# Optimization experiments

Hardware: AMD Instinct MI355X
Metric: run time of the kernel (lower is better)

The kernel has to match this reference:

```python
import jax, jax.numpy as jnp
import numpy as np

N = 100000   # num_nodes
E = 1250000  # num_edges
IN = 64
HID = 64
OUT = 64
LN_EPS = 1e-5


def _gcn_conv(x, src, dst, W, b, n):
    # PyG GCNConv: add self-loops, symmetric deg^{-1/2} normalization, then linear.
    h = x @ W  # (N, out)
    deg = jax.ops.segment_sum(jnp.ones(src.shape[0], h.dtype), dst, num_segments=n) + 1.0  # +1 self-loop
    dinv = jax.lax.rsqrt(deg)
    norm = dinv[src] * dinv[dst]  # (E,)
    out = jax.ops.segment_sum(h[src] * norm[:, None], dst, num_segments=n)
    out = out + h * (dinv * dinv)[:, None]  # self-loop message
    return out + b


def _sage_conv(x, src, dst, Wl, bl, Wr, n):
    # PyG SAGEConv(aggr='mean'): lin_l(mean_{j in N(i)} x_j) + lin_r(x_i); bias only in lin_l.
    cnt = jax.ops.segment_sum(jnp.ones(src.shape[0], x.dtype), dst, num_segments=n)
    agg = jax.ops.segment_sum(x[src], dst, num_segments=n) / jnp.maximum(cnt, 1.0)[:, None]
    return agg @ Wl + bl + x @ Wr


def _layer_norm(x, g, b):
    mu = jnp.mean(x, axis=-1, keepdims=True)
    var = jnp.var(x, axis=-1, keepdims=True)
    return (x - mu) * jax.lax.rsqrt(var + LN_EPS) * g + b


def setup_inputs() -> dict:
    key = jax.random.key(0)
    ks = jax.random.split(key, 16)
    def w(k, shape):
        fan_in = shape[0]
        return (jax.random.normal(k, shape, jnp.float32) / np.sqrt(fan_in)).astype(jnp.float32)
    x = jax.random.normal(ks[0], (N, IN), jnp.float32)
    edge_index = jax.random.randint(ks[1], (2, E), 0, N, dtype=jnp.int64)
    return {
        "x": x,
        "edge_index": edge_index,
        "gcn_w1": w(ks[2], (IN, HID)), "gcn_b1": jnp.zeros((HID,), jnp.float32),
        "gcn_w2": w(ks[3], (HID, OUT)), "gcn_b2": jnp.zeros((OUT,), jnp.float32),
        "sage_wl1": w(ks[4], (IN, HID)), "sage_bl1": jnp.zeros((HID,), jnp.float32),
        "sage_wr1": w(ks[5], (IN, HID)),
        "sage_wl2": w(ks[6], (HID, OUT)), "sage_bl2": jnp.zeros((OUT,), jnp.float32),
        "sage_wr2": w(ks[7], (HID, OUT)),
        "gcn_ln_g": jnp.ones((OUT,), jnp.float32), "gcn_ln_b": jnp.zeros((OUT,), jnp.float32),
        "sage_ln_g": jnp.ones((OUT,), jnp.float32), "sage_ln_b": jnp.zeros((OUT,), jnp.float32),
        "proj_w": w(ks[8], (2 * OUT, OUT)), "proj_b": jnp.zeros((OUT,), jnp.float32),
    }


def reference(x, edge_index, gcn_w1, gcn_b1, gcn_w2, gcn_b2,
              sage_wl1, sage_bl1, sage_wr1, sage_wl2, sage_bl2, sage_wr2,
              gcn_ln_g, gcn_ln_b, sage_ln_g, sage_ln_b, proj_w, proj_b):
    src, dst = edge_index[0], edge_index[1]
    n = x.shape[0]
    # GCN branch (dropout p=0 / eval -> identity)
    g = jax.nn.relu(_gcn_conv(x, src, dst, gcn_w1, gcn_b1, n))
    g = _gcn_conv(g, src, dst, gcn_w2, gcn_b2, n)
    # SAGE branch
    s = jax.nn.relu(_sage_conv(x, src, dst, sage_wl1, sage_bl1, sage_wr1, n))
    s = _sage_conv(s, src, dst, sage_wl2, sage_bl2, sage_wr2, n)
    # Norm + projected-concat fusion
    g = _layer_norm(g, gcn_ln_g, gcn_ln_b)
    s = _layer_norm(s, sage_ln_g, sage_ln_b)
    cat = jnp.concatenate([g, s], axis=-1)  # (N, 2*OUT)
    return cat @ proj_w + proj_b
```

## Files before the change

kernel.cpp:

```cpp
#include <hip/hip_runtime.h>


#define SCAN_CHUNK 2048

typedef __attribute__((ext_vector_type(8))) short short8;
typedef __attribute__((ext_vector_type(4))) short short4v;
typedef __attribute__((ext_vector_type(4))) float floatx4;

__device__ __forceinline__ unsigned short f2bf(float f) {
    unsigned int u = __float_as_uint(f);
    unsigned int r = u + 0x7FFFu + ((u >> 16) & 1u);
    return (unsigned short)(r >> 16);
}
__device__ __forceinline__ float bf2f(unsigned short h) {
    return __uint_as_float(((unsigned int)h) << 16);
}

__device__ __forceinline__ unsigned lds_addr(const void* p) {
    return (unsigned)(unsigned long long)(__attribute__((address_space(3))) const char*)p;
}

__device__ __forceinline__ short8 cat44(short4v lo, short4v hi) {
    short8 r;
    r[0] = lo[0]; r[1] = lo[1]; r[2] = lo[2]; r[3] = lo[3];
    r[4] = hi[0]; r[5] = hi[1]; r[6] = hi[2]; r[7] = hi[3];
    return r;
}

template<int NF, int CTB>
__device__ __forceinline__ void tr_read4(unsigned a0, short8 bf[4]) {
    short4v l0, h0, l1, h1, l2, h2, l3, h3;
    asm volatile(
        "ds_read_b64_tr_b16 %0, %8 offset:%9\n\t"
        "ds_read_b64_tr_b16 %1, %8 offset:%10\n\t"
        "ds_read_b64_tr_b16 %2, %8 offset:%11\n\t"
        "ds_read_b64_tr_b16 %3, %8 offset:%12\n\t"
        "ds_read_b64_tr_b16 %4, %8 offset:%13\n\t"
        "ds_read_b64_tr_b16 %5, %8 offset:%14\n\t"
        "ds_read_b64_tr_b16 %6, %8 offset:%15\n\t"
        "ds_read_b64_tr_b16 %7, %8 offset:%16\n\t"
        "s_waitcnt lgkmcnt(0)"
        : "=&v"(l0), "=&v"(h0), "=&v"(l1), "=&v"(h1),
          "=&v"(l2), "=&v"(h2), "=&v"(l3), "=&v"(h3)
        : "v"(a0),
          "i"((0 * NF + CTB + 0) * 128), "i"((1 * NF + CTB + 0) * 128),
          "i"((0 * NF + CTB + 1) * 128), "i"((1 * NF + CTB + 1) * 128),
          "i"((0 * NF + CTB + 2) * 128), "i"((1 * NF + CTB + 2) * 128),
          "i"((0 * NF + CTB + 3) * 128), "i"((1 * NF + CTB + 3) * 128)
        : "memory");
    bf[0] = cat44(l0, h0);
    bf[1] = cat44(l1, h1);
    bf[2] = cat44(l2, h2);
    bf[3] = cat44(l3, h3);
}

__global__ void k_count(const int* __restrict__ ei, int E, int* __restrict__ cnt,
                        int* __restrict__ rank,
                        const float* __restrict__ x, unsigned short* __restrict__ xb,
                        int xtotal, int do_x) {
    int i = blockIdx.x * blockDim.x + threadIdx.x;
    int e = i * 8;
    if (e + 8 <= E) {
        int4 d0 = *(const int4*)&ei[E + e];
        int4 d1 = *(const int4*)&ei[E + e + 4];
        int4 r0, r1;
        r0.x = atomicAdd(&cnt[d0.x], 1);
        r0.y = atomicAdd(&cnt[d0.y], 1);
        r0.z = atomicAdd(&cnt[d0.z], 1);
        r0.w = atomicAdd(&cnt[d0.w], 1);
        r1.x = atomicAdd(&cnt[d1.x], 1);
        r1.y = atomicAdd(&cnt[d1.y], 1);
        r1.z = atomicAdd(&cnt[d1.z], 1);
        r1.w = atomicAdd(&cnt[d1.w], 1);
        *(int4*)&rank[e] = r0;
        *(int4*)&rank[e + 4] = r1;
    } else if (e < E) {
        for (int j = e; j < E; ++j) rank[j] = atomicAdd(&cnt[ei[E + j]], 1);
    }
    if (do_x) {
        int xe = i * 8;
        if (xe + 8 <= xtotal) {
            float4 a = *(const float4*)&x[xe];
            float4 b = *(const float4*)&x[xe + 4];
            short8 o;
            o[0] = (short)f2bf(a.x); o[1] = (short)f2bf(a.y);
            o[2] = (short)f2bf(a.z); o[3] = (short)f2bf(a.w);
            o[4] = (short)f2bf(b.x); o[5] = (short)f2bf(b.y);
            o[6] = (short)f2bf(b.z); o[7] = (short)f2bf(b.w);
            *(short8*)&xb[xe] = o;
        } else if (xe < xtotal) {
            for (int j = xe; j < xtotal; ++j) xb[j] = f2bf(x[j]);
        }
    }
}

__global__ void k_scan_reduce(const int* __restrict__ cnt, int N, int* __restrict__ blockSums) {
    __shared__ int lds[256];
    int base = blockIdx.x * SCAN_CHUNK;
    int t = threadIdx.x;
    int s = 0;
    for (int j = 0; j < 8; ++j) {
        int idx = base + t * 8 + j;
        if (idx < N) s += cnt[idx] + 1;
    }
    lds[t] = s;
    __syncthreads();
    for (int d = 128; d > 0; d >>= 1) {
        if (t < d) lds[t] += lds[t + d];
        __syncthreads();
    }
    if (t == 0) blockSums[blockIdx.x] = lds[0];
}

__global__ void k_scan_spine(int* __restrict__ blockSums, int B) {
    if (threadIdx.x == 0 && blockIdx.x == 0) {
        int run = 0;
        for (int b = 0; b < B; ++b) { int v = blockSums[b]; blockSums[b] = run; run += v; }
    }
}

__global__ void k_scan_write(const int* __restrict__ cnt, int N,
                             const int* __restrict__ blockSums,
                             int* __restrict__ offs, float* __restrict__ dinv) {
    __shared__ int lds[256];
    int base = blockIdx.x * SCAN_CHUNK;
    int t = threadIdx.x;
    int v[8];
    int s = 0;
    for (int j = 0; j < 8; ++j) {
        int idx = base + t * 8 + j;
        v[j] = (idx < N) ? cnt[idx] : 0;
        s += (idx < N) ? v[j] + 1 : 0;
    }
    lds[t] = s;
    __syncthreads();
    for (int d = 1; d < 256; d <<= 1) {
        int x = (t >= d) ? lds[t - d] : 0;
        __syncthreads();
        lds[t] += x;
        __syncthreads();
    }
    int excl = (t == 0) ? 0 : lds[t - 1];
    int run = blockSums[blockIdx.x] + excl;
    for (int j = 0; j < 8; ++j) {
        int idx = base + t * 8 + j;
        if (idx < N) {
            offs[idx] = run;
            run += v[j] + 1;
            dinv[idx] = rsqrtf((float)v[j] + 1.0f);
            if (idx == N - 1) offs[N] = run;
        }
    }
}

__global__ void k_fill(const int* __restrict__ ei, int E, const int* __restrict__ offs,
                       const int* __restrict__ rank, const int* __restrict__ cnt,
                       const float* __restrict__ dinv,
                       int* __restrict__ csr, unsigned int* __restrict__ pk,
                       int use_pk, int N) {
    int i = blockIdx.x * blockDim.x + threadIdx.x;
    int e = i * 8;
    if (e + 8 <= E) {
        int4 s0 = *(const int4*)&ei[e];
        int4 s1 = *(const int4*)&ei[e + 4];
        int4 d0 = *(const int4*)&ei[E + e];
        int4 d1 = *(const int4*)&ei[E + e + 4];
        int4 r0 = *(const int4*)&rank[e];
        int4 r1 = *(const int4*)&rank[e + 4];
        int p0 = offs[d0.x] + r0.x, p1 = offs[d0.y] + r0.y;
        int p2 = offs[d0.z] + r0.z, p3 = offs[d0.w] + r0.w;
        int p4 = offs[d1.x] + r1.x, p5 = offs[d1.y] + r1.y;
        int p6 = offs[d1.z] + r1.z, p7 = offs[d1.w] + r1.w;
        csr[p0] = s0.x; csr[p1] = s0.y; csr[p2] = s0.z; csr[p3] = s0.w;
        csr[p4] = s1.x; csr[p5] = s1.y; csr[p6] = s1.z; csr[p7] = s1.w;
        if (use_pk) {
            pk[p0] = ((unsigned)(d0.x & 15) << 16) | f2bf(dinv[s0.x] * dinv[d0.x]);
            pk[p1] = ((unsigned)(d0.y & 15) << 16) | f2bf(dinv[s0.y] * dinv[d0.y]);
            pk[p2] = ((unsigned)(d0.z & 15) << 16) | f2bf(dinv[s0.z] * dinv[d0.z]);
            pk[p3] = ((unsigned)(d0.w & 15) << 16) | f2bf(dinv[s0.w] * dinv[d0.w]);
            pk[p4] = ((unsigned)(d1.x & 15) << 16) | f2bf(dinv[s1.x] * dinv[d1.x]);
            pk[p5] = ((unsigned)(d1.y & 15) << 16) | f2bf(dinv[s1.y] * dinv[d1.y]);
            pk[p6] = ((unsigned)(d1.z & 15) << 16) | f2bf(dinv[s1.z] * dinv[d1.z]);
            pk[p7] = ((unsigned)(d1.w & 15) << 16) | f2bf(dinv[s1.w] * dinv[d1.w]);
        }
    } else if (e < E) {
        for (int j = e; j < E; ++j) {
            int dd = ei[E + j];
            int p = offs[dd] + rank[j];
            csr[p] = ei[j];
            if (use_pk) pk[p] = ((unsigned)(dd & 15) << 16) | f2bf(dinv[ei[j]] * dinv[dd]);
        }
    }
    if (use_pk && i < N) {
        int pos = offs[i] + cnt[i];
        float di = dinv[i];
        csr[pos] = i;
        pk[pos] = ((unsigned)(i & 15) << 16) | (1u << 20) | f2bf(di * di);
    }
}

template<int ROWSH>
__launch_bounds__(256)
__global__ void k_gatherM(const unsigned short* __restrict__ feat,
                          const int* __restrict__ csr,
                          const unsigned int* __restrict__ pk,
                          const int* __restrict__ offs, const int* __restrict__ cnt,
                          unsigned short* __restrict__ agg, int N) {
    constexpr int NF = ROWSH / 16;
    constexpr int LPR = ROWSH / 8;
    constexpr int EPP = 64 / LPR;
    constexpr int PASSES = 32 / EPP;

    __shared__ unsigned short sbuf[4][32 * ROWSH];

    const int lane = threadIdx.x & 63;
    const int wv = threadIdx.x >> 6;
    const int base = blockIdx.x * 64 + wv * 16;
    if (base >= N) return;

    const int q = lane >> 4;
    const int d16 = lane & 15;

    const int parity = lane & 1;
    const int ei_low = (lane >> 1) & 3;
    const int sf_sub = (lane >> 3) & (NF - 1);
    const int ei_high = (NF == 8) ? 0 : (lane >> 5);
    const int eid = ei_high * 4 + ei_low;
    const int sf = sf_sub * 16 + parity * 8;

    const int elo = offs[base];
    const int ehi = offs[min(base + 16, N)];
    const int emax = ehi - 1;
    const int nch = (ehi - elo + 31) >> 5;

    int cM0, cM1, cM2, cM3;
    unsigned pM0, pM1, pM2, pM3;
    {
        int i0 = elo + lane;
        int i1 = i0 + 64, i2 = i0 + 128, i3 = i0 + 192;
        cM0 = csr[i0 <= emax ? i0 : emax];
        cM1 = csr[i1 <= emax ? i1 : emax];
        cM2 = csr[i2 <= emax ? i2 : emax];
        cM3 = csr[i3 <= emax ? i3 : emax];
        unsigned t0 = pk[i0 <= emax ? i0 : emax];
        unsigned t1 = pk[i1 <= emax ? i1 : emax];
        unsigned t2 = pk[i2 <= emax ? i2 : emax];
        unsigned t3 = pk[i3 <= emax ? i3 : emax];
        pM0 = (i0 < ehi) ? t0 : 0x00100000u;
        pM1 = (i1 < ehi) ? t1 : 0x00100000u;
        pM2 = (i2 < ehi) ? t2 : 0x00100000u;
        pM3 = (i3 < ehi) ? t3 : 0x00100000u;
    }

    floatx4 accg[4], accs[4];
#pragma unroll
    for (int i = 0; i < 4; ++i) {
        accg[i] = floatx4{0.f, 0.f, 0.f, 0.f};
        accs[i] = floatx4{0.f, 0.f, 0.f, 0.f};
    }

    unsigned short* wb = &sbuf[wv][0];
    const unsigned a0 = lds_addr(wb) + (unsigned)(q * 2 * NF) * 128u + (unsigned)d16 * 8u;

    for (int c = 0; c < nch; ++c) {
        int cv; unsigned pv; int wofs;
        int rc = c >> 1;
        if (rc < 4) {
            wofs = (c & 1) << 5;
            cv = (rc == 0) ? cM0 : (rc == 1) ? cM1 : (rc == 2) ? cM2 : cM3;
            pv = (rc == 0) ? pM0 : (rc == 1) ? pM1 : (rc == 2) ? pM2 : pM3;
        } else {
            int idx = elo + (c << 5) + lane;
            int idc = idx <= emax ? idx : emax;
            cv = csr[idc];
            unsigned t = pk[idc];
            pv = (idx < ehi) ? t : 0x00100000u;
            wofs = 0;
        }

        short8 stg[PASSES];
#pragma unroll
        for (int p = 0; p < PASSES; ++p) {
            int src = __shfl(cv, wofs + p * EPP + eid, 64);
            stg[p] = *(const short8*)&feat[(size_t)src * ROWSH + sf];
        }

        short8 aG, aS;
#pragma unroll
        for (int j = 0; j < 8; ++j) {
            unsigned u = (unsigned)__shfl((int)pv, wofs + q * 8 + j, 64);
            unsigned hi = u >> 16;
            bool match = (int)(hi & 15u) == d16;
            aG[j] = match ? (short)(u & 0xFFFFu) : (short)0;
            aS[j] = (match && !(hi & 16u)) ? (short)0x3F80 : (short)0;
        }

#pragma unroll
        for (int p = 0; p < PASSES; ++p)
            *(short8*)&wb[p * 512 + lane * 8] = stg[p];
        asm volatile("s_waitcnt lgkmcnt(0)" ::: "memory");
        __builtin_amdgcn_sched_barrier(0);

        short8 bG[4];
        tr_read4<NF, 0>(a0, bG);
#pragma unroll
        for (int ct = 0; ct < 4; ++ct)
            accg[ct] = __builtin_amdgcn_mfma_f32_16x16x32_bf16(aG, bG[ct], accg[ct], 0, 0, 0);
        if constexpr (NF == 8) {
            short8 bS[4];
            tr_read4<NF, 4>(a0, bS);
#pragma unroll
            for (int ct = 0; ct < 4; ++ct)
                accs[ct] = __builtin_amdgcn_mfma_f32_16x16x32_bf16(aS, bS[ct], accs[ct], 0, 0, 0);
        } else {
#pragma unroll
            for (int ct = 0; ct < 4; ++ct)
                accs[ct] = __builtin_amdgcn_mfma_f32_16x16x32_bf16(aS, bG[ct], accs[ct], 0, 0, 0);
        }
    }

#pragma unroll
    for (int r = 0; r < 4; ++r) {
        int node = base + q * 4 + r;
        if (node < N) {
            float rn = 1.0f / fmaxf((float)cnt[node], 1.0f);
#pragma unroll
            for (int ct = 0; ct < 4; ++ct) {
                agg[(size_t)node * 128 + ct * 16 + d16]      = f2bf(accg[ct][r]);
                agg[(size_t)node * 128 + 64 + ct * 16 + d16] = f2bf(accs[ct][r] * rn);
            }
        }
    }
}

__device__ __forceinline__ void xor_reduce8(float4& a, float4& b) {
    a.x += __shfl_xor(a.x, 16, 64); a.y += __shfl_xor(a.y, 16, 64);
    a.z += __shfl_xor(a.z, 16, 64); a.w += __shfl_xor(a.w, 16, 64);
    b.x += __shfl_xor(b.x, 16, 64); b.y += __shfl_xor(b.y, 16, 64);
    b.z += __shfl_xor(b.z, 16, 64); b.w += __shfl_xor(b.w, 16, 64);
    a.x += __shfl_xor(a.x, 32, 64); a.y += __shfl_xor(a.y, 32, 64);
    a.z += __shfl_xor(a.z, 32, 64); a.w += __shfl_xor(a.w, 32, 64);
    b.x += __shfl_xor(b.x, 32, 64); b.y += __shfl_xor(b.y, 32, 64);
    b.z += __shfl_xor(b.z, 32, 64); b.w += __shfl_xor(b.w, 32, 64);
}

__device__ __forceinline__ float red16(float v) {
    v += __shfl_xor(v, 1, 64);
    v += __shfl_xor(v, 2, 64);
    v += __shfl_xor(v, 4, 64);
    v += __shfl_xor(v, 8, 64);
    return v;
}

__global__ void k_gather1_f32(const float* __restrict__ x, const int* __restrict__ csr,
                              const int* __restrict__ offs, const int* __restrict__ cnt,
                              const float* __restrict__ dinv,
                              unsigned short* __restrict__ agg, int N) {
    int lane = threadIdx.x & 63;
    int wave = threadIdx.x >> 6;
    int node = blockIdx.x * 4 + wave;
    if (node >= N) return;
    int c = lane & 15, grp = lane >> 4;

    int st = offs[node];
    int cn = cnt[node];
    float di = dinv[node];

    float4 aA = {0.f, 0.f, 0.f, 0.f}, aB = {0.f, 0.f, 0.f, 0.f};
    for (int e = 0; e < cn; e += 8) {
        int i0 = e + grp, i1 = e + 4 + grp;
        float m0 = (i0 < cn) ? 1.f : 0.f;
        float m1 = (i1 < cn) ? 1.f : 0.f;
        int s0 = csr[st + (i0 < cn ? i0 : cn - 1)];
        int s1 = csr[st + (i1 < cn ? i1 : cn - 1)];
        float w0 = m0 * dinv[s0];
        float w1 = m1 * dinv[s1];
        float4 v0 = *(const float4*)&x[(size_t)s0 * 64 + 4 * c];
        float4 v1 = *(const float4*)&x[(size_t)s1 * 64 + 4 * c];
        aA.x += w0 * v0.x + w1 * v1.x; aA.y += w0 * v0.y + w1 * v1.y;
        aA.z += w0 * v0.z + w1 * v1.z; aA.w += w0 * v0.w + w1 * v1.w;
        aB.x += m0 * v0.x + m1 * v1.x; aB.y += m0 * v0.y + m1 * v1.y;
        aB.z += m0 * v0.z + m1 * v1.z; aB.w += m0 * v0.w + m1 * v1.w;
    }
    xor_reduce8(aA, aB);

    if (grp == 0) {
        float4 sq = *(const float4*)&x[(size_t)node * 64 + 4 * c];
        float d2 = di * di;
        ushort4 o;
        o.x = f2bf(di * aA.x + d2 * sq.x); o.y = f2bf(di * aA.y + d2 * sq.y);
        o.z = f2bf(di * aA.z + d2 * sq.z); o.w = f2bf(di * aA.w + d2 * sq.w);
        *(ushort4*)&agg[(size_t)node * 128 + 4 * c] = o;
    } else if (grp == 1) {
        float rn = 1.0f / fmaxf((float)cn, 1.0f);
        ushort4 o;
        o.x = f2bf(aB.x * rn); o.y = f2bf(aB.y * rn);
        o.z = f2bf(aB.z * rn); o.w = f2bf(aB.w * rn);
        *(ushort4*)&agg[(size_t)node * 128 + 64 + 4 * c] = o;
    }
}

__global__ void k_gather2(const unsigned short* __restrict__ gs, const int* __restrict__ csr,
                          const int* __restrict__ offs, const int* __restrict__ cnt,
                          const float* __restrict__ dinv,
                          unsigned short* __restrict__ agg, int N) {
    int lane = threadIdx.x & 63;
    int wave = threadIdx.x >> 6;
    int node = blockIdx.x * 4 + wave;
    if (node >= N) return;
    int c = lane & 15, grp = lane >> 4;

    int st = offs[node];
    int cn = cnt[node];
    float di = dinv[node];

    float4 aC = {0.f, 0.f, 0.f, 0.f}, aD = {0.f, 0.f, 0.f, 0.f};
    for (int e = 0; e < cn; e += 8) {
        int i0 = e + grp, i1 = e + 4 + grp;
        float m0 = (i0 < cn) ? 1.f : 0.f;
        float m1 = (i1 < cn) ? 1.f : 0.f;
        int s0 = csr[st + (i0 < cn ? i0 : cn - 1)];
        int s1 = csr[st + (i1 < cn ? i1 : cn - 1)];
        float w0 = m0 * dinv[s0];
        float w1 = m1 * dinv[s1];
        const unsigned short* p0 = gs + (size_t)s0 * 128 + 4 * c;
        const unsigned short* p1 = gs + (size_t)s1 * 128 + 4 * c;
        ushort4 g0u = *(const ushort4*)p0;
        ushort4 g1u = *(const ushort4*)p1;
        ushort4 t0u = *(const ushort4*)(p0 + 64);
        ushort4 t1u = *(const ushort4*)(p1 + 64);
        aC.x += w0 * bf2f(g0u.x) + w1 * bf2f(g1u.x);
        aC.y += w0 * bf2f(g0u.y) + w1 * bf2f(g1u.y);
        aC.z += w0 * bf2f(g0u.z) + w1 * bf2f(g1u.z);
        aC.w += w0 * bf2f(g0u.w) + w1 * bf2f(g1u.w);
        aD.x += m0 * bf2f(t0u.x) + m1 * bf2f(t1u.x);
        aD.y += m0 * bf2f(t0u.y) + m1 * bf2f(t1u.y);
        aD.z += m0 * bf2f(t0u.z) + m1 * bf2f(t1u.z);
        aD.w += m0 * bf2f(t0u.w) + m1 * bf2f(t1u.w);
    }
    xor_reduce8(aC, aD);

    if (grp == 0) {
        ushort4 su = *(const ushort4*)&gs[(size_t)node * 128 + 4 * c];
        float d2 = di * di;
        ushort4 o;
        o.x = f2bf(di * aC.x + d2 * bf2f(su.x));
        o.y = f2bf(di * aC.y + d2 * bf2f(su.y));
        o.z = f2bf(di * aC.z + d2 * bf2f(su.z));
        o.w = f2bf(di * aC.w + d2 * bf2f(su.w));
        *(ushort4*)&agg[(size_t)node * 128 + 4 * c] = o;
    } else if (grp == 1) {
        float rn = 1.0f / fmaxf((float)cn, 1.0f);
        ushort4 o;
        o.x = f2bf(aD.x * rn); o.y = f2bf(aD.y * rn);
        o.z = f2bf(aD.z * rn); o.w = f2bf(aD.w * rn);
        *(ushort4*)&agg[(size_t)node * 128 + 64 + 4 * c] = o;
    }
}

__launch_bounds__(512, 1)
__global__ void k_gemm1(const unsigned short* __restrict__ agg,
                        const unsigned short* __restrict__ xb,
                        const float* __restrict__ xf, int use_xb,
                        const float* __restrict__ W1, const float* __restrict__ b1,
                        const float* __restrict__ Wl1, const float* __restrict__ bl1,
                        const float* __restrict__ Wr1,
                        unsigned short* __restrict__ buf1, int N) {
    alignas(16) __shared__ unsigned short sW[3][4096];
    int t = threadIdx.x;
    for (int i = t; i < 1536; i += 512) {
        int m = i >> 9;
        int rem = i & 511;
        int f = rem >> 6;
        int L = rem & 63;
        int kb = (f >> 2) * 32 + (L >> 4) * 8;
        int o = (f & 3) * 16 + (L & 15);
        const float* Wsrc = (m == 0) ? W1 : (m == 1) ? Wl1 : Wr1;
        unsigned short* dst = &sW[m][f * 512 + L * 8];
        #pragma unroll
        for (int j = 0; j < 8; ++j) dst[j] = f2bf(Wsrc[(kb + j) * 64 + o]);
    }
    __syncthreads();

    int lane = t & 63;
    int wave = t >> 6;
    int quad = lane >> 4;
    int n16 = lane & 15;
    int base = blockIdx.x * 128 + wave * 16;
    if (base >= N) return;

    int nm = base + n16;
    if (nm >= N) nm = N - 1;
    const unsigned short* ar = agg + (size_t)nm * 128;

    {
        short8 a0 = *(const short8*)(ar + quad * 8);
        short8 a1 = *(const short8*)(ar + 32 + quad * 8);
        floatx4 g0 = {0.f, 0.f, 0.f, 0.f}, g1 = g0, g2 = g0, g3 = g0;
        g0 = __builtin_amdgcn_mfma_f32_16x16x32_bf16(a0, *(const short8*)&sW[0][0 * 512 + lane * 8], g0, 0, 0, 0);
        g0 = __builtin_amdgcn_mfma_f32_16x16x32_bf16(a1, *(const short8*)&sW[0][4 * 512 + lane * 8], g0, 0, 0, 0);
        g1 = __builtin_amdgcn_mfma_f32_16x16x32_bf16(a0, *(const short8*)&sW[0][1 * 512 + lane * 8], g1, 0, 0, 0);
        g1 = __builtin_amdgcn_mfma_f32_16x16x32_bf16(a1, *(const short8*)&sW[0][5 * 512 + lane * 8], g1, 0, 0, 0);
        g2 = __builtin_amdgcn_mfma_f32_16x16x32_bf16(a0, *(const short8*)&sW[0][2 * 512 + lane * 8], g2, 0, 0, 0);
        g2 = __builtin_amdgcn_mfma_f32_16x16x32_bf16(a1, *(const short8*)&sW[0][6 * 512 + lane * 8], g2, 0, 0, 0);
        g3 = __builtin_amdgcn_mfma_f32_16x16x32_bf16(a0, *(const short8*)&sW[0][3 * 512 + lane * 8], g3, 0, 0, 0);
        g3 = __builtin_amdgcn_mfma_f32_16x16x32_bf16(a1, *(const short8*)&sW[0][7 * 512 + lane * 8], g3, 0, 0, 0);
        floatx4 gt[4] = {g0, g1, g2, g3};
        #pragma unroll
        for (int nt = 0; nt < 4; ++nt) {
            float bg = b1[nt * 16 + n16];
            #pragma unroll
            for (int r = 0; r < 4; ++r) {
                int node = base + quad * 4 + r;
                if (node < N)
                    buf1[(size_t)node * 128 + nt * 16 + n16] = f2bf(fmaxf(gt[nt][r] + bg, 0.f));
            }
        }
    }

    {
        short8 a0 = *(const short8*)(ar + 64 + quad * 8);
        short8 a1 = *(const short8*)(ar + 96 + quad * 8);
        short8 ax0, ax1;
        if (use_xb) {
            ax0 = *(const short8*)&xb[(size_t)nm * 64 + quad * 8];
            ax1 = *(const short8*)&xb[(size_t)nm * 64 + 32 + quad * 8];
        } else {
            float4 xq0 = *(const float4*)&xf[(size_t)nm * 64 + quad * 8];
            float4 xq1 = *(const float4*)&xf[(size_t)nm * 64 + quad * 8 + 4];
            float4 xq2 = *(const float4*)&xf[(size_t)nm * 64 + 32 + quad * 8];
            float4 xq3 = *(const float4*)&xf[(size_t)nm * 64 + 32 + quad * 8 + 4];
            ax0[0] = (short)f2bf(xq0.x); ax0[1] = (short)f2bf(xq0.y);
            ax0[2] = (short)f2bf(xq0.z); ax0[3] = (short)f2bf(xq0.w);
            ax0[4] = (short)f2bf(xq1.x); ax0[5] = (short)f2bf(xq1.y);
            ax0[6] = (short)f2bf(xq1.z); ax0[7] = (short)f2bf(xq1.w);
            ax1[0] = (short)f2bf(xq2.x); ax1[1] = (short)f2bf(xq2.y);
            ax1[2] = (short)f2bf(xq2.z); ax1[3] = (short)f2bf(xq2.w);
            ax1[4] = (short)f2bf(xq3.x); ax1[5] = (short)f2bf(xq3.y);
            ax1[6] = (short)f2bf(xq3.z); ax1[7] = (short)f2bf(xq3.w);
        }

        floatx4 s0 = {0.f, 0.f, 0.f, 0.f}, s1 = s0, s2 = s0, s3 = s0;
        s0 = __builtin_amdgcn_mfma_f32_16x16x32_bf16(a0, *(const short8*)&sW[1][0 * 512 + lane * 8], s0, 0, 0, 0);
        s0 = __builtin_amdgcn_mfma_f32_16x16x32_bf16(a1, *(const short8*)&sW[1][4 * 512 + lane * 8], s0, 0, 0, 0);
        s0 = __builtin_amdgcn_mfma_f32_16x16x32_bf16(ax0, *(const short8*)&sW[2][0 * 512 + lane * 8], s0, 0, 0, 0);
        s0 = __builtin_amdgcn_mfma_f32_16x16x32_bf16(ax1, *(const short8*)&sW[2][4 * 512 + lane * 8], s0, 0, 0, 0);
        s1 = __builtin_amdgcn_mfma_f32_16x16x32_bf16(a0, *(const short8*)&sW[1][1 * 512 + lane * 8], s1, 0, 0, 0);
        s1 = __builtin_amdgcn_mfma_f32_16x16x32_bf16(a1, *(const short8*)&sW[1][5 * 512 + lane * 8], s1, 0, 0, 0);
        s1 = __builtin_amdgcn_mfma_f32_16x16x32_bf16(ax0, *(const short8*)&sW[2][1 * 512 + lane * 8], s1, 0, 0, 0);
        s1 = __builtin_amdgcn_mfma_f32_16x16x32_bf16(ax1, *(const short8*)&sW[2][5 * 512 + lane * 8], s1, 0, 0, 0);
        s2 = __builtin_amdgcn_mfma_f32_16x16x32_bf16(a0, *(const short8*)&sW[1][2 * 512 + lane * 8], s2, 0, 0, 0);
        s2 = __builtin_amdgcn_mfma_f32_16x16x32_bf16(a1, *(const short8*)&sW[1][6 * 512 + lane * 8], s2, 0, 0, 0);
        s2 = __builtin_amdgcn_mfma_f32_16x16x32_bf16(ax0, *(const short8*)&sW[2][2 * 512 + lane * 8], s2, 0, 0, 0);
        s2 = __builtin_amdgcn_mfma_f32_16x16x32_bf16(ax1, *(const short8*)&sW[2][6 * 512 + lane * 8], s2, 0, 0, 0);
        s3 = __builtin_amdgcn_mfma_f32_16x16x32_bf16(a0, *(const short8*)&sW[1][3 * 512 + lane * 8], s3, 0, 0, 0);
        s3 = __builtin_amdgcn_mfma_f32_16x16x32_bf16(a1, *(const short8*)&sW[1][7 * 512 + lane * 8], s3, 0, 0, 0);
        s3 = __builtin_amdgcn_mfma_f32_16x16x32_bf16(ax0, *(const short8*)&sW[2][3 * 512 + lane * 8], s3, 0, 0, 0);
        s3 = __builtin_amdgcn_mfma_f32_16x16x32_bf16(ax1, *(const short8*)&sW[2][7 * 512 + lane * 8], s3, 0, 0, 0);
        floatx4 stl[4] = {s0, s1, s2, s3};
        #pragma unroll
        for (int nt = 0; nt < 4; ++nt) {
            float bs = bl1[nt * 16 + n16];
            #pragma unroll
            for (int r = 0; r < 4; ++r) {
                int node = base + quad * 4 + r;
                if (node < N)
                    buf1[(size_t)node * 128 + 64 + nt * 16 + n16] = f2bf(fmaxf(stl[nt][r] + bs, 0.f));
            }
        }
    }
}

__launch_bounds__(512, 1)
__global__ void k_gemm2(const unsigned short* __restrict__ agg,
                        const unsigned short* __restrict__ buf1,
                        const float* __restrict__ W2, const float* __restrict__ b2,
                        const float* __restrict__ Wl2, const float* __restrict__ bl2,
                        const float* __restrict__ Wr2,
                        const float* __restrict__ lngG, const float* __restrict__ lnbG,
                        const float* __restrict__ lngS, const float* __restrict__ lnbS,
                        const float* __restrict__ Pw, const float* __restrict__ Pb,
                        float* __restrict__ out, int N) {
    alignas(16) __shared__ unsigned short sW[3][4096];
    alignas(16) __shared__ unsigned short sP[8192];
    alignas(16) __shared__ unsigned short sT[8][16 * 132];
    int t = threadIdx.x;
    for (int i = t; i < 1536; i += 512) {
        int m = i >> 9;
        int rem = i & 511;
        int f = rem >> 6;
        int L = rem & 63;
        int kb = (f >> 2) * 32 + (L >> 4) * 8;
        int o = (f & 3) * 16 + (L & 15);
        const float* Wsrc = (m == 0) ? W2 : (m == 1) ? Wl2 : Wr2;
        unsigned short* dst = &sW[m][f * 512 + L * 8];
        #pragma unroll
        for (int j = 0; j < 8; ++j) dst[j] = f2bf(Wsrc[(kb + j) * 64 + o]);
    }
    for (int i = t; i < 1024; i += 512) {
        int f = i >> 6;
        int L = i & 63;
        int kb = (f >> 2) * 32 + (L >> 4) * 8;
        int o = (f & 3) * 16 + (L & 15);
        unsigned short* dst = &sP[f * 512 + L * 8];
        #pragma unroll
        for (int j = 0; j < 8; ++j) dst[j] = f2bf(Pw[(kb + j) * 64 + o]);
    }
    __syncthreads();

    int lane = t & 63;
    int wave = t >> 6;
    int quad = lane >> 4;
    int n16 = lane & 15;
    int base = blockIdx.x * 128 + wave * 16;
    if (base >= N) return;
    int nm = base + n16;
    if (nm >= N) nm = N - 1;
    const unsigned short* ar = agg + (size_t)nm * 128;
    const unsigned short* br = buf1 + (size_t)nm * 128;
    unsigned short* tw = &sT[wave][0];

    {
        short8 a0 = *(const short8*)(ar + quad * 8);
        short8 a1 = *(const short8*)(ar + 32 + quad * 8);
        floatx4 c0 = {0.f, 0.f, 0.f, 0.f}, c1 = c0, c2 = c0, c3 = c0;
        c0 = __builtin_amdgcn_mfma_f32_16x16x32_bf16(a0, *(const short8*)&sW[0][0 * 512 + lane * 8], c0, 0, 0, 0);
        c0 = __builtin_amdgcn_mfma_f32_16x16x32_bf16(a1, *(const short8*)&sW[0][4 * 512 + lane * 8], c0, 0, 0, 0);
        c1 = __builtin_amdgcn_mfma_f32_16x16x32_bf16(a0, *(const short8*)&sW[0][1 * 512 + lane * 8], c1, 0, 0, 0);
        c1 = __builtin_amdgcn_mfma_f32_16x16x32_bf16(a1, *(const short8*)&sW[0][5 * 512 + lane * 8], c1, 0, 0, 0);
        c2 = __builtin_amdgcn_mfma_f32_16x16x32_bf16(a0, *(const short8*)&sW[0][2 * 512 + lane * 8], c2, 0, 0, 0);
        c2 = __builtin_amdgcn_mfma_f32_16x16x32_bf16(a1, *(const short8*)&sW[0][6 * 512 + lane * 8], c2, 0, 0, 0);
        c3 = __builtin_amdgcn_mfma_f32_16x16x32_bf16(a0, *(const short8*)&sW[0][3 * 512 + lane * 8], c3, 0, 0, 0);
        c3 = __builtin_amdgcn_mfma_f32_16x16x32_bf16(a1, *(const short8*)&sW[0][7 * 512 + lane * 8], c3, 0, 0, 0);

        float bv0 = b2[n16], bv1 = b2[16 + n16], bv2 = b2[32 + n16], bv3 = b2[48 + n16];
        float gv0 = lngG[n16], gv1 = lngG[16 + n16], gv2 = lngG[32 + n16], gv3 = lngG[48 + n16];
        float ev0 = lnbG[n16], ev1 = lnbG[16 + n16], ev2 = lnbG[32 + n16], ev3 = lnbG[48 + n16];
        #pragma unroll
        for (int r = 0; r < 4; ++r) {
            float z0 = c0[r] + bv0, z1 = c1[r] + bv1, z2 = c2[r] + bv2, z3 = c3[r] + bv3;
            float s = red16(z0 + z1 + z2 + z3);
            float q = red16(z0 * z0 + z1 * z1 + z2 * z2 + z3 * z3);
            float mu = s * (1.0f / 64.0f);
            float var = fmaxf(q * (1.0f / 64.0f) - mu * mu, 0.0f);
            float rs = rsqrtf(var + 1e-5f);
            unsigned short* row = tw + (quad * 4 + r) * 132;
            row[n16]      = f2bf((z0 - mu) * rs * gv0 + ev0);
            row[16 + n16] = f2bf((z1 - mu) * rs * gv1 + ev1);
            row[32 + n16] = f2bf((z2 - mu) * rs * gv2 + ev2);
            row[48 + n16] = f2bf((z3 - mu) * rs * gv3 + ev3);
        }
    }

    {
        short8 a0 = *(const short8*)(ar + 64 + quad * 8);
        short8 a1 = *(const short8*)(ar + 96 + quad * 8);
        short8 v0 = *(const short8*)(br + 64 + quad * 8);
        short8 v1 = *(const short8*)(br + 96 + quad * 8);
        floatx4 c0 = {0.f, 0.f, 0.f, 0.f}, c1 = c0, c2 = c0, c3 = c0;
        c0 = __builtin_amdgcn_mfma_f32_16x16x32_bf16(a0, *(const short8*)&sW[1][0 * 512 + lane * 8], c0, 0, 0, 0);
        c0 = __builtin_amdgcn_mfma_f32_16x16x32_bf16(a1, *(const short8*)&sW[1][4 * 512 + lane * 8], c0, 0, 0, 0);
        c0 = __builtin_amdgcn_mfma_f32_16x16x32_bf16(v0, *(const short8*)&sW[2][0 * 512 + lane * 8], c0, 0, 0, 0);
        c0 = __builtin_amdgcn_mfma_f32_16x16x32_bf16(v1, *(const short8*)&sW[2][4 * 512 + lane * 8], c0, 0, 0, 0);
        c1 = __builtin_amdgcn_mfma_f32_16x16x32_bf16(a0, *(const short8*)&sW[1][1 * 512 + lane * 8], c1, 0, 0, 0);
        c1 = __builtin_amdgcn_mfma_f32_16x16x32_bf16(a1, *(const short8*)&sW[1][5 * 512 + lane * 8], c1, 0, 0, 0);
        c1 = __builtin_amdgcn_mfma_f32_16x16x32_bf16(v0, *(const short8*)&sW[2][1 * 512 + lane * 8], c1, 0, 0, 0);
        c1 = __builtin_amdgcn_mfma_f32_16x16x32_bf16(v1, *(const short8*)&sW[2][5 * 512 + lane * 8], c1, 0, 0, 0);
        c2 = __builtin_amdgcn_mfma_f32_16x16x32_bf16(a0, *(const short8*)&sW[1][2 * 512 + lane * 8], c2, 0, 0, 0);
        c2 = __builtin_amdgcn_mfma_f32_16x16x32_bf16(a1, *(const short8*)&sW[1][6 * 512 + lane * 8], c2, 0, 0, 0);
        c2 = __builtin_amdgcn_mfma_f32_16x16x32_bf16(v0, *(const short8*)&sW[2][2 * 512 + lane * 8], c2, 0, 0, 0);
        c2 = __builtin_amdgcn_mfma_f32_16x16x32_bf16(v1, *(const short8*)&sW[2][6 * 512 + lane * 8], c2, 0, 0, 0);
        c3 = __builtin_amdgcn_mfma_f32_16x16x32_bf16(a0, *(const short8*)&sW[1][3 * 512 + lane * 8], c3, 0, 0, 0);
        c3 = __builtin_amdgcn_mfma_f32_16x16x32_bf16(a1, *(const short8*)&sW[1][7 * 512 + lane * 8], c3, 0, 0, 0);
        c3 = __builtin_amdgcn_mfma_f32_16x16x32_bf16(v0, *(const short8*)&sW[2][3 * 512 + lane * 8], c3, 0, 0, 0);
        c3 = __builtin_amdgcn_mfma_f32_16x16x32_bf16(v1, *(const short8*)&sW[2][7 * 512 + lane * 8], c3, 0, 0, 0);

        float bv0 = bl2[n16], bv1 = bl2[16 + n16], bv2 = bl2[32 + n16], bv3 = bl2[48 + n16];
        float gv0 = lngS[n16], gv1 = lngS[16 + n16], gv2 = lngS[32 + n16], gv3 = lngS[48 + n16];
        float ev0 = lnbS[n16], ev1 = lnbS[16 + n16], ev2 = lnbS[32 + n16], ev3 = lnbS[48 + n16];
        #pragma unroll
        for (int r = 0; r < 4; ++r) {
            float z0 = c0[r] + bv0, z1 = c1[r] + bv1, z2 = c2[r] + bv2, z3 = c3[r] + bv3;
            float s = red16(z0 + z1 + z2 + z3);
            float q = red16(z0 * z0 + z1 * z1 + z2 * z2 + z3 * z3);
            float mu = s * (1.0f / 64.0f);
            float var = fmaxf(q * (1.0f / 64.0f) - mu * mu, 0.0f);
            float rs = rsqrtf(var + 1e-5f);
            unsigned short* row = tw + (quad * 4 + r) * 132 + 64;
            row[n16]      = f2bf((z0 - mu) * rs * gv0 + ev0);
            row[16 + n16] = f2bf((z1 - mu) * rs * gv1 + ev1);
            row[32 + n16] = f2bf((z2 - mu) * rs * gv2 + ev2);
            row[48 + n16] = f2bf((z3 - mu) * rs * gv3 + ev3);
        }
    }

    floatx4 o0 = {0.f, 0.f, 0.f, 0.f}, o1 = o0, o2 = o0, o3 = o0;
    #pragma unroll
    for (int ks = 0; ks < 4; ++ks) {
        const unsigned short* ap = tw + n16 * 132 + ks * 32 + quad * 8;
        short4v lo = *(const short4v*)ap;
        short4v hi = *(const short4v*)(ap + 4);
        short8 af;
        af[0] = lo[0]; af[1] = lo[1]; af[2] = lo[2]; af[3] = lo[3];
        af[4] = hi[0]; af[5] = hi[1]; af[6] = hi[2]; af[7] = hi[3];
        o0 = __builtin_amdgcn_mfma_f32_16x16x32_bf16(af, *(const short8*)&sP[(ks * 4 + 0) * 512 + lane * 8], o0, 0, 0, 0);
        o1 = __builtin_amdgcn_mfma_f32_16x16x32_bf16(af, *(const short8*)&sP[(ks * 4 + 1) * 512 + lane * 8], o1, 0, 0, 0);
        o2 = __builtin_amdgcn_mfma_f32_16x16x32_bf16(af, *(const short8*)&sP[(ks * 4 + 2) * 512 + lane * 8], o2, 0, 0, 0);
        o3 = __builtin_amdgcn_mfma_f32_16x16x32_bf16(af, *(const short8*)&sP[(ks * 4 + 3) * 512 + lane * 8], o3, 0, 0, 0);
    }
    float p0 = Pb[n16], p1 = Pb[16 + n16], p2 = Pb[32 + n16], p3 = Pb[48 + n16];
    floatx4 ot[4] = {o0, o1, o2, o3};
    float pv[4] = {p0, p1, p2, p3};
    #pragma unroll
    for (int nt = 0; nt < 4; ++nt) {
        #pragma unroll
        for (int r = 0; r < 4; ++r) {
            int node = base + quad * 4 + r;
            if (node < N) out[(size_t)node * 64 + nt * 16 + n16] = ot[nt][r] + pv[nt];
        }
    }
}

extern "C" void kernel_launch(void* const* d_in, const int* in_sizes, int n_in,
                              void* d_out, int out_size, void* d_ws, size_t ws_size,
                              hipStream_t stream) {
    const float* x        = (const float*)d_in[0];
    const int*   ei       = (const int*)d_in[1];
    const float* gcn_w1   = (const float*)d_in[2];
    const float* gcn_b1   = (const float*)d_in[3];
    const float* gcn_w2   = (const float*)d_in[4];
    const float* gcn_b2   = (const float*)d_in[5];
    const float* sage_wl1 = (const float*)d_in[6];
    const float* sage_bl1 = (const float*)d_in[7];
    const float* sage_wr1 = (const float*)d_in[8];
    const float* sage_wl2 = (const float*)d_in[9];
    const float* sage_bl2 = (const float*)d_in[10];
    const float* sage_wr2 = (const float*)d_in[11];
    const float* gcn_ln_g = (const float*)d_in[12];
    const float* gcn_ln_b = (const float*)d_in[13];
    const float* sage_ln_g = (const float*)d_in[14];
    const float* sage_ln_b = (const float*)d_in[15];
    const float* proj_w   = (const float*)d_in[16];
    const float* proj_b   = (const float*)d_in[17];
    float* out = (float*)d_out;

    const int N = in_sizes[0] / 64;
    const int E = in_sizes[1] / 2;
    const int B = (N + SCAN_CHUNK - 1) / SCAN_CHUNK;

    char* w = (char*)d_ws;
    size_t off = 0;
    auto alloc = [&](size_t bytes) -> void* {
        void* p = w + off;
        off = (off + bytes + 255) & ~(size_t)255;
        return p;
    };
    int*            cnt       = (int*)alloc((size_t)N * 4);
    int*            offs      = (int*)alloc((size_t)(N + 1) * 4);
    float*          dinv      = (float*)alloc((size_t)N * 4);
    int*            blockSums = (int*)alloc((size_t)(B + 1) * 4);
    int*            csr       = (int*)alloc((size_t)(E + N + 64) * 4);
    unsigned short* agg       = (unsigned short*)alloc((size_t)N * 128 * 2);
    unsigned short* buf1      = (unsigned short*)alloc((size_t)N * 128 * 2);
    size_t off_nonew = off;
    unsigned int*   pk        = (unsigned int*)alloc((size_t)(E + N + 64) * 4);
    unsigned short* xb        = (unsigned short*)alloc((size_t)N * 64 * 2);
    int use_new = (off <= ws_size) ? 1 : 0;
    if (!use_new) off = off_nonew;
    int* rank = (int*)agg;
    (void)n_in; (void)out_size;

    hipMemsetAsync(cnt, 0, (size_t)N * 4, stream);

    int e8Blocks = ((E + 7) / 8 + 255) / 256;
    int x8Blocks = ((N * 64 + 7) / 8 + 255) / 256;
    int cntBlocks = use_new ? max(e8Blocks, x8Blocks) : e8Blocks;
    int fillBlocks = use_new ? max(e8Blocks, (N + 255) / 256) : e8Blocks;
    k_count<<<cntBlocks, 256, 0, stream>>>(ei, E, cnt, rank, x, xb, N * 64, use_new);
    k_scan_reduce<<<B, 256, 0, stream>>>(cnt, N, blockSums);
    k_scan_spine<<<1, 64, 0, stream>>>(blockSums, B);
    k_scan_write<<<B, 256, 0, stream>>>(cnt, N, blockSums, offs, dinv);
    k_fill<<<fillBlocks, 256, 0, stream>>>(ei, E, offs, rank, cnt, dinv, csr, pk, use_new, N);

    if (use_new) {
        k_gatherM<64><<<(N + 63) / 64, 256, 0, stream>>>(xb, csr, pk, offs, cnt, agg, N);
        k_gemm1<<<(N + 127) / 128, 512, 0, stream>>>(agg, xb, x, 1, gcn_w1, gcn_b1,
                                                     sage_wl1, sage_bl1, sage_wr1, buf1, N);
        k_gatherM<128><<<(N + 63) / 64, 256, 0, stream>>>(buf1, csr, pk, offs, cnt, agg, N);
    } else {
        k_gather1_f32<<<(N + 3) / 4, 256, 0, stream>>>(x, csr, offs, cnt, dinv, agg, N);
        k_gemm1<<<(N + 127) / 128, 512, 0, stream>>>(agg, xb, x, 0, gcn_w1, gcn_b1,
                                                     sage_wl1, sage_bl1, sage_wr1, buf1, N);
        k_gather2<<<(N + 3) / 4, 256, 0, stream>>>(buf1, csr, offs, cnt, dinv, agg, N);
    }
    k_gemm2<<<(N + 127) / 128, 512, 0, stream>>>(agg, buf1, gcn_w2, gcn_b2,
                                                 sage_wl2, sage_bl2, sage_wr2,
                                                 gcn_ln_g, gcn_ln_b, sage_ln_g, sage_ln_b,
                                                 proj_w, proj_b, out, N);
}
```

Measured before the change: 337.6 us.

## Privatize degree counters per XCD to localize atomics in CSR build

Degree counting now uses eight per-XCD counter arrays, indexed by the hardware XCC id, with workgroup-scope relaxed atomics. The rank is encoded together with the XCD id. The scan sums the eight arrays to get the totals and writes a per-XCD base offset table that the fill kernel uses to place edges. The aim is to avoid cross-die atomic contention and coherence traffic on a single shared counter array, at the cost of 8x larger counter memsets and scan reads. Workgroup-scope atomics on global memory shared by several CUs within an XCD depend on the L2 handling them, so correctness relies on that hardware behaviour.

New measurement: 364.2 us. +7.9%, slower.

```diff
diff --git a/kernel.cpp b/kernel.cpp
--- a/kernel.cpp
+++ b/kernel.cpp
@@ -18,6 +18,12 @@
 
 __device__ __forceinline__ unsigned lds_addr(const void* p) {
     return (unsigned)(unsigned long long)(__attribute__((address_space(3))) const char*)p;
+}
+
+__device__ __forceinline__ int get_xcc() {
+    int x;
+    asm("s_getreg_b32 %0, hwreg(20, 0, 32)" : "=s"(x));
+    return x & 7;
 }
 
 __device__ __forceinline__ short8 cat44(short4v lo, short4v hi) {
@@ -54,28 +60,38 @@
     bf[3] = cat44(l3, h3);
 }
 
-__global__ void k_count(const int* __restrict__ ei, int E, int* __restrict__ cnt,
+__global__ void k_count(const int* __restrict__ ei, int E,
+                        unsigned int* __restrict__ cnt8, int N,
                         int* __restrict__ rank,
                         const float* __restrict__ x, unsigned short* __restrict__ xb,
                         int xtotal, int do_x) {
+    int xcd = get_xcc();
+    unsigned int* myc = cnt8 + (size_t)xcd * N;
     int i = blockIdx.x * blockDim.x + threadIdx.x;
     int e = i * 8;
     if (e + 8 <= E) {
         int4 d0 = *(const int4*)&ei[E + e];
         int4 d1 = *(const int4*)&ei[E + e + 4];
         int4 r0, r1;
-        r0.x = atomicAdd(&cnt[d0.x], 1);
-        r0.y = atomicAdd(&cnt[d0.y], 1);
-        r0.z = atomicAdd(&cnt[d0.z], 1);
-        r0.w = atomicAdd(&cnt[d0.w], 1);
-        r1.x = atomicAdd(&cnt[d1.x], 1);
-        r1.y = atomicAdd(&cnt[d1.y], 1);
-        r1.z = atomicAdd(&cnt[d1.z], 1);
-        r1.w = atomicAdd(&cnt[d1.w], 1);
+        r0.x = (int)__hip_atomic_fetch_add(&myc[d0.x], 1u, __ATOMIC_RELAXED, __HIP_MEMORY_SCOPE_WORKGROUP);
+        r0.y = (int)__hip_atomic_fetch_add(&myc[d0.y], 1u, __ATOMIC_RELAXED, __HIP_MEMORY_SCOPE_WORKGROUP);
+        r0.z = (int)__hip_atomic_fetch_add(&myc[d0.z], 1u, __ATOMIC_RELAXED, __HIP_MEMORY_SCOPE_WORKGROUP);
+        r0.w = (int)__hip_atomic_fetch_add(&myc[d0.w], 1u, __ATOMIC_RELAXED, __HIP_MEMORY_SCOPE_WORKGROUP);
+        r1.x = (int)__hip_atomic_fetch_add(&myc[d1.x], 1u, __ATOMIC_RELAXED, __HIP_MEMORY_SCOPE_WORKGROUP);
+        r1.y = (int)__hip_atomic_fetch_add(&myc[d1.y], 1u, __ATOMIC_RELAXED, __HIP_MEMORY_SCOPE_WORKGROUP);
+        r1.z = (int)__hip_atomic_fetch_add(&myc[d1.z], 1u, __ATOMIC_RELAXED, __HIP_MEMORY_SCOPE_WORKGROUP);
+        r1.w = (int)__hip_atomic_fetch_add(&myc[d1.w], 1u, __ATOMIC_RELAXED, __HIP_MEMORY_SCOPE_WORKGROUP);
+        r0.x = (r0.x << 3) | xcd; r0.y = (r0.y << 3) | xcd;
+        r0.z = (r0.z << 3) | xcd; r0.w = (r0.w << 3) | xcd;
+        r1.x = (r1.x << 3) | xcd; r1.y = (r1.y << 3) | xcd;
+        r1.z = (r1.z << 3) | xcd; r1.w = (r1.w << 3) | xcd;
         *(int4*)&rank[e] = r0;
         *(int4*)&rank[e + 4] = r1;
     } else if (e < E) {
-        for (int j = e; j < E; ++j) rank[j] = atomicAdd(&cnt[ei[E + j]], 1);
+        for (int j = e; j < E; ++j) {
+            int rl = (int)__hip_atomic_fetch_add(&myc[ei[E + j]], 1u, __ATOMIC_RELAXED, __HIP_MEMORY_SCOPE_WORKGROUP);
+            rank[j] = (rl << 3) | xcd;
+        }
     }
     if (do_x) {
         int xe = i * 8;
@@ -94,14 +110,20 @@
     }
 }
 
-__global__ void k_scan_reduce(const int* __restrict__ cnt, int N, int* __restrict__ blockSums) {
+__global__ void k_scan_reduce(const unsigned int* __restrict__ cnt8, int N,
+                              int* __restrict__ blockSums) {
     __shared__ int lds[256];
     int base = blockIdx.x * SCAN_CHUNK;
     int t = threadIdx.x;
     int s = 0;
     for (int j = 0; j < 8; ++j) {
         int idx = base + t * 8 + j;
-        if (idx < N) s += cnt[idx] + 1;
+        if (idx < N) {
+            int tot = 0;
+            #pragma unroll
+            for (int k = 0; k < 8; ++k) tot += (int)cnt8[(size_t)k * N + idx];
+            s += tot + 1;
+        }
     }
     lds[t] = s;
     __syncthreads();
@@ -119,9 +141,10 @@
     }
 }
 
-__global__ void k_scan_write(const int* __restrict__ cnt, int N,
+__global__ void k_scan_write(const unsigned int* __restrict__ cnt8, int N,
                              const int* __restrict__ blockSums,
-                             int* __restrict__ offs, float* __restrict__ dinv) {
+                             int* __restrict__ offs, int* __restrict__ cnt,
+                             float* __restrict__ dinv, int* __restrict__ boff8) {
     __shared__ int lds[256];
     int base = blockIdx.x * SCAN_CHUNK;
     int t = threadIdx.x;
@@ -129,8 +152,13 @@
     int s = 0;
     for (int j = 0; j < 8; ++j) {
         int idx = base + t * 8 + j;
-        v[j] = (idx < N) ? cnt[idx] : 0;
-        s += (idx < N) ? v[j] + 1 : 0;
+        int tot = 0;
+        if (idx < N) {
+            #pragma unroll
+            for (int k = 0; k < 8; ++k) tot += (int)cnt8[(size_t)k * N + idx];
+        }
+        v[j] = tot;
+        s += (idx < N) ? tot + 1 : 0;
     }
     lds[t] = s;
     __syncthreads();
@@ -146,6 +174,13 @@
         int idx = base + t * 8 + j;
         if (idx < N) {
             offs[idx] = run;
+            cnt[idx] = v[j];
+            int acc = run;
+            #pragma unroll
+            for (int k = 0; k < 8; ++k) {
+                boff8[(size_t)k * N + idx] = acc;
+                acc += (int)cnt8[(size_t)k * N + idx];
+            }
             run += v[j] + 1;
             dinv[idx] = rsqrtf((float)v[j] + 1.0f);
             if (idx == N - 1) offs[N] = run;
@@ -155,9 +190,9 @@
 
 __global__ void k_fill(const int* __restrict__ ei, int E, const int* __restrict__ offs,
                        const int* __restrict__ rank, const int* __restrict__ cnt,
+                       const int* __restrict__ boff8, int N,
                        const float* __restrict__ dinv,
-                       int* __restrict__ csr, unsigned int* __restrict__ pk,
-                       int use_pk, int N) {
+                       int* __restrict__ csr, unsigned int* __restrict__ pk, int use_pk) {
     int i = blockIdx.x * blockDim.x + threadIdx.x;
     int e = i * 8;
     if (e + 8 <= E) {
@@ -167,10 +202,14 @@
         int4 d1 = *(const int4*)&ei[E + e + 4];
         int4 r0 = *(const int4*)&rank[e];
         int4 r1 = *(const int4*)&rank[e + 4];
-        int p0 = offs[d0.x] + r0.x, p1 = offs[d0.y] + r0.y;
-        int p2 = offs[d0.z] + r0.z, p3 = offs[d0.w] + r0.w;
-        int p4 = offs[d1.x] + r1.x, p5 = offs[d1.y] + r1.y;
-        int p6 = offs[d1.z] + r1.z, p7 = offs[d1.w] + r1.w;
+        int p0 = boff8[(size_t)(r0.x & 7) * N + d0.x] + (r0.x >> 3);
+        int p1 = boff8[(size_t)(r0.y & 7) * N + d0.y] + (r0.y >> 3);
+        int p2 = boff8[(size_t)(r0.z & 7) * N + d0.z] + (r0.z >> 3);
+        int p3 = boff8[(size_t)(r0.w & 7) * N + d0.w] + (r0.w >> 3);
+        int p4 = boff8[(size_t)(r1.x & 7) * N + d1.x] + (r1.x >> 3);
+        int p5 = boff8[(size_t)(r1.y & 7) * N + d1.y] + (r1.y >> 3);
+        int p6 = boff8[(size_t)(r1.z & 7) * N + d1.z] + (r1.z >> 3);
+        int p7 = boff8[(size_t)(r1.w & 7) * N + d1.w] + (r1.w >> 3);
         csr[p0] = s0.x; csr[p1] = s0.y; csr[p2] = s0.z; csr[p3] = s0.w;
         csr[p4] = s1.x; csr[p5] = s1.y; csr[p6] = s1.z; csr[p7] = s1.w;
         if (use_pk) {
@@ -186,7 +225,8 @@
     } else if (e < E) {
         for (int j = e; j < E; ++j) {
             int dd = ei[E + j];
-            int p = offs[dd] + rank[j];
+            int r = rank[j];
+            int p = boff8[(size_t)(r & 7) * N + dd] + (r >> 3);
             csr[p] = ei[j];
             if (use_pk) pk[p] = ((unsigned)(dd & 15) << 16) | f2bf(dinv[ei[j]] * dinv[dd]);
         }
@@ -760,6 +800,8 @@
     float*          dinv      = (float*)alloc((size_t)N * 4);
     int*            blockSums = (int*)alloc((size_t)(B + 1) * 4);
     int*            csr       = (int*)alloc((size_t)(E + N + 64) * 4);
+    unsigned int*   cnt8      = (unsigned int*)alloc((size_t)8 * N * 4);
+    int*            boff8     = (int*)alloc((size_t)8 * N * 4);
     unsigned short* agg       = (unsigned short*)alloc((size_t)N * 128 * 2);
     unsigned short* buf1      = (unsigned short*)alloc((size_t)N * 128 * 2);
     size_t off_nonew = off;
@@ -770,17 +812,17 @@
     int* rank = (int*)agg;
     (void)n_in; (void)out_size;
 
-    hipMemsetAsync(cnt, 0, (size_t)N * 4, stream);
+    hipMemsetAsync(cnt8, 0, (size_t)8 * N * 4, stream);
 
     int e8Blocks = ((E + 7) / 8 + 255) / 256;
     int x8Blocks = ((N * 64 + 7) / 8 + 255) / 256;
     int cntBlocks = use_new ? max(e8Blocks, x8Blocks) : e8Blocks;
     int fillBlocks = use_new ? max(e8Blocks, (N + 255) / 256) : e8Blocks;
-    k_count<<<cntBlocks, 256, 0, stream>>>(ei, E, cnt, rank, x, xb, N * 64, use_new);
-    k_scan_reduce<<<B, 256, 0, stream>>>(cnt, N, blockSums);
+    k_count<<<cntBlocks, 256, 0, stream>>>(ei, E, cnt8, N, rank, x, xb, N * 64, use_new);
+    k_scan_reduce<<<B, 256, 0, stream>>>(cnt8, N, blockSums);
     k_scan_spine<<<1, 64, 0, stream>>>(blockSums, B);
-    k_scan_write<<<B, 256, 0, stream>>>(cnt, N, blockSums, offs, dinv);
-    k_fill<<<fillBlocks, 256, 0, stream>>>(ei, E, offs, rank, cnt, dinv, csr, pk, use_new, N);
+    k_scan_write<<<B, 256, 0, stream>>>(cnt8, N, blockSums, offs, cnt, dinv, boff8);
+    k_fill<<<fillBlocks, 256, 0, stream>>>(ei, E, offs, rank, cnt, boff8, N, dinv, csr, pk, use_new);
 
     if (use_new) {
         k_gatherM<64><<<(N + 63) / 64, 256, 0, stream>>>(xb, csr, pk, offs, cnt, agg, N);
```
